# Kernel tuning notes

Hardware: AMD Instinct MI355X
Metric: run time of the kernel (lower is better)

Reference implementation:

```python
import jax, jax.numpy as jnp
import numpy as np

B, DIM, W0, H0 = 4, 256, 128, 128
HEADS, HEAD_DIM = 8, 32
FOLD, PROP = 2, 4
EPS_GN = 1e-5


def _l2norm(x):
    n = jnp.linalg.norm(x, axis=-1, keepdims=True)
    return x / jnp.maximum(n, 1e-12)  # matches F.normalize eps


def _fold(t, f):
    # (b, c, f*w, f*h) -> (b*f*f, c, w, h), matching einops '(b f1 f2)' ordering
    b, c, W, H = t.shape
    w, h = W // f, H // f
    return t.reshape(b, c, f, w, f, h).transpose(0, 2, 4, 1, 3, 5).reshape(b * f * f, c, w, h)


def _unfold(t, f, b0):
    bf, c, w, h = t.shape
    return t.reshape(b0, f, f, c, w, h).transpose(0, 3, 1, 4, 2, 5).reshape(b0, c, f * w, f * h)


def _pool(t, p):
    # AdaptiveAvgPool2d((p, p)) for divisible sizes
    b, c, w, h = t.shape
    return t.reshape(b, c, p, w // p, p, h // p).mean(axis=(3, 5))


def setup_inputs() -> dict:
    key = jax.random.key(0)
    ks = jax.random.split(key, 6)
    D = HEADS * HEAD_DIM
    return {
        "x": jax.random.normal(ks[0], (B, DIM, W0, H0), jnp.float32),
        "xyz": jax.random.normal(ks[1], (B, 3, W0, H0), jnp.float32),
        "Wv": jax.random.normal(ks[2], (D, DIM, 7, 7), jnp.float32) * 0.02,
        "bv": jnp.zeros((D,), jnp.float32),
        "Wproj": jax.random.normal(ks[3], (DIM, D), jnp.float32) * 0.02,
        "bproj": jnp.zeros((DIM,), jnp.float32),
        "gn_w": jnp.ones((D,), jnp.float32),
        "gn_b": jnp.zeros((D,), jnp.float32),
        "sim_alpha": jnp.ones((1,), jnp.float32),
        "sim_beta": jnp.zeros((1,), jnp.float32),
    }


def reference(x, xyz, Wv, bv, Wproj, bproj, gn_w, gn_b, sim_alpha, sim_beta):
    # value = self.v(x): 7x7 conv, padding 3
    value = jax.lax.conv_general_dilated(
        x, Wv, (1, 1), ((3, 3), (3, 3)),
        dimension_numbers=("NCHW", "OIHW", "NCHW")) + bv[None, :, None, None]
    b0 = x.shape[0]
    # heads split: 'b (e c) w h -> (b e) c w h'
    xh = x.reshape(b0 * HEADS, HEAD_DIM, W0, H0)
    vh = value.reshape(b0 * HEADS, HEAD_DIM, W0, H0)
    xf = _fold(xh, FOLD)
    vf = _fold(vh, FOLD)
    xyzf = _fold(xyz, FOLD)
    bb, c, w, h = xf.shape
    M = PROP * PROP
    N = w * h
    centers = _pool(xf, PROP)                                   # (bb, c, p, p)
    xyz_c = _pool(xyzf, PROP)
    value_centers = _pool(vf, PROP).reshape(bb, c, M).transpose(0, 2, 1)  # (bb, M, c)
    cen = centers.reshape(bb, c, M).transpose(0, 2, 1)          # (bb, M, c)
    xpts = xf.reshape(bb, c, N).transpose(0, 2, 1)              # (bb, N, c)
    vpts = vf.reshape(bb, c, N).transpose(0, 2, 1)              # (bb, N, c)
    sim = jax.nn.sigmoid(sim_beta + sim_alpha *
                         jnp.einsum('bmc,bnc->bmn', _l2norm(cen), _l2norm(xpts)))
    bg = xyzf.shape[0]
    xyz_pts = xyzf.reshape(bg, 3, N).transpose(0, 2, 1)
    xyz_cc = xyz_c.reshape(bg, 3, M).transpose(0, 2, 1)
    sim_geo = jax.nn.sigmoid(sim_beta + sim_alpha *
                             jnp.einsum('bmc,bnc->bmn', _l2norm(xyz_cc), _l2norm(xyz_pts)))
    sim_geo = jnp.tile(sim_geo, (sim.shape[0] // sim_geo.shape[0], 1, 1))  # torch .repeat
    sim = sim * sim_geo ** 2
    # faithful mask math: scatter_(1, argmax, 1.0) into an all-ones tensor leaves it all-ones,
    # so dense_mask == 1 and split_mask == 0 exactly as in the source.
    dense_mask = jnp.ones_like(sim)
    split_mask = 1.0 - dense_mask
    denss_sim = sim * dense_mask
    split_sim = sim * split_mask
    split_out = (jnp.einsum('bmn,bnc->bmc', split_sim, vpts) + value_centers) \
                / (split_sim.sum(-1, keepdims=True) + 1.0)
    denss_out = (jnp.einsum('bmn,bnc->bmc', denss_sim, xpts) + cen) \
                / (denss_sim.sum(-1, keepdims=True) + 1.0)
    denss_pts = jnp.einsum('bmc,bmn->bnc', denss_out, denss_sim)  # (bb, N, c)
    split_pts = jnp.einsum('bmc,bmn->bnc', split_out, split_sim)
    out = (denss_pts + split_pts).transpose(0, 2, 1).reshape(bb, c, w, h)
    out = _unfold(out, FOLD, b0 * HEADS)
    out = out.reshape(b0, HEADS * HEAD_DIM, W0, H0)
    # GroupNorm with 1 group: normalize over (C, H, W) per sample
    mu = out.mean(axis=(1, 2, 3), keepdims=True)
    var = ((out - mu) ** 2).mean(axis=(1, 2, 3), keepdims=True)
    out = (out - mu) / jnp.sqrt(var + EPS_GN)
    out = out * gn_w[None, :, None, None] + gn_b[None, :, None, None]
    # proj 1x1 conv + silu
    out = jnp.einsum('bchw,oc->bohw', out, Wproj) + bproj[None, :, None, None]
    return jax.nn.silu(out)
```

## Files before the change

### kernel.cpp

```cpp
#include <hip/hip_runtime.h>
#include <stdint.h>


typedef __attribute__((ext_vector_type(8))) short short8;
typedef __attribute__((ext_vector_type(4))) float floatx4;
typedef __fp16 fp16x2 __attribute__((ext_vector_type(2)));

#define SIMW 264

__device__ float g_sbp[256];
__device__ float g_bias[1024];
__device__ __attribute__((aligned(16))) _Float16 g_Wa[4*256*256];
__device__ float g_cenraw[128*16*32];
__device__ float g_cenhat[128*16*32];
__device__ float g_gcenhat[16*16*4];
__device__ __attribute__((aligned(16))) _Float16 g_sim[(size_t)128*4096*16];
__device__ float g_dnum[128*16*16*32];
__device__ float g_Gp[(size_t)128*16*256];
__device__ float g_rsum[128*16*16];
__device__ __attribute__((aligned(16))) unsigned g_dnh2[128*256];

static __device__ __forceinline__ fp16x2 as_h2(unsigned u) { return __builtin_bit_cast(fp16x2, u); }
static __device__ __forceinline__ unsigned pk(float a, float b) {
  return __builtin_bit_cast(unsigned, __builtin_amdgcn_cvt_pkrtz(a, b));
}
static __device__ __forceinline__ float h16(float v) {
  return (float)as_h2(pk(v, 0.f))[0];
}
#if __has_builtin(__builtin_amdgcn_fdot2)
static __device__ __forceinline__ float fdot2(fp16x2 a, fp16x2 b, float c) {
  return __builtin_amdgcn_fdot2(a, b, c, false);
}
#else
static __device__ __forceinline__ float fdot2(fp16x2 a, fp16x2 b, float c) {
  return c + (float)a[0]*(float)b[0] + (float)a[1]*(float)b[1];
}
#endif
static __device__ __forceinline__ float sum16(const float* p) {
  const float4* q = (const float4*)p;
  float4 a = q[0], b = q[1], c = q[2], d = q[3];
  return (a.x+a.y+a.z+a.w) + (b.x+b.y+b.z+b.w) + (c.x+c.y+c.z+c.w) + (d.x+d.y+d.z+d.w);
}
static __device__ __forceinline__ float sigm(float z) {
  return __builtin_amdgcn_rcpf(1.f + __expf(-z));
}

__global__ __launch_bounds__(128) void k01_pool(const float* __restrict__ x,
                                                const float* __restrict__ xyz) {
  __shared__ float cenL[128];
  __shared__ float invL[4];
  __shared__ float gc[64];
  const int blk = blockIdx.x;
  const int tid = threadIdx.x;
  if (blk < 512) {
    const int bb = blk >> 2, pi = blk & 3;
    const int b = bb >> 5, e = (bb >> 2) & 7, f1 = (bb >> 1) & 1, f2 = bb & 1;
    const int c = tid >> 2, pj = tid & 3;
    const int m = pi*4 + pj;
    const float* p = x + ((size_t)(b*256 + e*32 + c)*128 + f1*64 + pi*16)*128 + f2*64 + pj*16;
    float s = 0.f;
    #pragma unroll
    for (int r = 0; r < 16; ++r) s += sum16(p + r*128);
    const float raw = s * (1.f/256.f);
    cenL[pj*32 + c] = raw;
    g_cenraw[(bb*16 + m)*32 + c] = raw;
    __syncthreads();
    if (tid < 4) {
      float ss = 0.f;
      #pragma unroll
      for (int cc = 0; cc < 32; ++cc) { float v = cenL[tid*32+cc]; ss += v*v; }
      invL[tid] = 1.f / fmaxf(sqrtf(ss), 1e-12f);
    }
    __syncthreads();
    g_cenhat[(bb*16 + m)*32 + c] = raw * invL[pj];
  } else {
    const int gti = blk - 512;
    const int bg = gti >> 2, f1 = (gti >> 1) & 1, f2 = gti & 1;
    if (tid < 48) {
      const int m = tid / 3, ch = tid - 3*(tid/3);
      const int pi = m >> 2, pj = m & 3;
      const float* p = xyz + (size_t)(bg*3+ch)*16384 + (f1*64 + pi*16)*128 + f2*64 + pj*16;
      float s = 0.f;
      #pragma unroll
      for (int r = 0; r < 16; ++r) s += sum16(p + r*128);
      gc[m*4+ch] = s * (1.f/256.f);
    }
    __syncthreads();
    if (tid < 16) {
      float g0 = gc[tid*4], g1 = gc[tid*4+1], g2 = gc[tid*4+2];
      float inv = 1.f / fmaxf(sqrtf(g0*g0+g1*g1+g2*g2), 1e-12f);
      float* o = g_gcenhat + gti*64 + tid*4;
      o[0] = g0*inv; o[1] = g1*inv; o[2] = g2*inv; o[3] = 0.f;
    }
  }
}

__global__ __launch_bounds__(256, 5) void k1b_sim(const float* __restrict__ x,
                                                  const float* __restrict__ xyz,
                                                  const float* __restrict__ salpha,
                                                  const float* __restrict__ sbeta) {
  __shared__ __attribute__((aligned(16))) unsigned  xL[256*20];
  __shared__ __attribute__((aligned(16))) _Float16 simS[16*SIMW];
  __shared__ __attribute__((aligned(16))) unsigned chP[16*16];
  __shared__ float gcenL[64];
  __shared__ float rsW[64];
  float* ovl = (float*)xL;
  const int blk = blockIdx.x;
  const int bb = blk >> 4, ck = blk & 15;
  const int b = bb >> 5, e = (bb >> 2) & 7, f1 = (bb >> 1) & 1, f2 = bb & 1;
  const int gti = ((e & 3) << 2) | (f1 << 1) | f2;
  const int tid = threadIdx.x, lane = tid & 63, wave = tid >> 6;
  const int lm = lane & 15, quad = lane >> 4;
  const float alpha = salpha[0], beta = sbeta[0];
  const float* xt = x + (((size_t)(b*256 + e*32))*128 + f1*64)*128 + f2*64;

  {
    const float2 cp = *(const float2*)(g_cenhat + bb*512 + tid*2);
    chP[tid] = pk(cp.x, cp.y);
  }
  if (tid < 64) gcenL[tid] = g_gcenhat[gti*64 + tid];
  __syncthreads();

  const int ng = ck*256 + tid;
  const int wi = ng >> 6, hi = ng & 63;
  const int addr = wi*128 + hi;
  {
    float ss = 0.f;
    unsigned xp[16];
    #pragma unroll
    for (int p = 0; p < 16; ++p) {
      const float v0 = xt[(size_t)(2*p)*16384 + addr];
      const float v1 = xt[(size_t)(2*p+1)*16384 + addr];
      ss += v0*v0 + v1*v1;
      xp[p] = pk(v0, v1);
    }
    uint4 u0 = {xp[0],xp[1],xp[2],xp[3]};
    uint4 u1 = {xp[4],xp[5],xp[6],xp[7]};
    uint4 u2 = {xp[8],xp[9],xp[10],xp[11]};
    uint4 u3 = {xp[12],xp[13],xp[14],xp[15]};
    *(uint4*)(xL + tid*20)      = u0;
    *(uint4*)(xL + tid*20 + 4)  = u1;
    *(uint4*)(xL + tid*20 + 8)  = u2;
    *(uint4*)(xL + tid*20 + 12) = u3;
    const float invn = __builtin_amdgcn_rcpf(fmaxf(sqrtf(ss), 1e-12f));
    const float* gp = xyz + (size_t)((e & 3)*3)*16384 + (f1*64 + wi)*128 + f2*64 + hi;
    float g0 = gp[0], g1 = gp[16384], g2 = gp[32768];
    const float invg = __builtin_amdgcn_rcpf(fmaxf(sqrtf(g0*g0+g1*g1+g2*g2), 1e-12f));
    float4 tail = {invn, g0*invg, g1*invg, g2*invg};
    *(float4*)((float*)xL + tid*20 + 16) = tail;
  }
  __syncthreads();

  {
    const short8 afx = *(const short8*)((const _Float16*)chP + lm*32 + quad*8);
    float rsacc[4] = {0.f, 0.f, 0.f, 0.f};
    #pragma unroll
    for (int t = 0; t < 4; ++t) {
      const int px = wave*64 + t*16 + lm;
      const short8 bfx = *(const short8*)((const _Float16*)xL + px*40 + quad*8);
      floatx4 d = {0.f,0.f,0.f,0.f};
      d = __builtin_amdgcn_mfma_f32_16x16x32_f16(afx, bfx, d, 0, 0, 0);
      const float4 ig = *(const float4*)((const float*)xL + px*20 + 16);
      #pragma unroll
      for (int r = 0; r < 4; ++r) {
        const int m = quad*4 + r;
        const float* gh = gcenL + m*4;
        const float dg = gh[0]*ig.y + gh[1]*ig.z + gh[2]*ig.w;
        const float gg = sigm(beta + alpha*dg);
        const float sv = sigm(beta + alpha * d[r] * ig.x) * gg * gg;
        rsacc[r] += sv;
        simS[m*SIMW + px] = (_Float16)sv;
      }
    }
    #pragma unroll
    for (int r = 0; r < 4; ++r) {
      float v = rsacc[r];
      v += __shfl_xor(v, 1, 64); v += __shfl_xor(v, 2, 64);
      v += __shfl_xor(v, 4, 64); v += __shfl_xor(v, 8, 64);
      if (lm == 0) rsW[wave*16 + quad*4 + r] = v;
    }
  }
  __syncthreads();

  {
    unsigned w[8];
    const unsigned short* sp = (const unsigned short*)simS;
    #pragma unroll
    for (int p = 0; p < 8; ++p)
      w[p] = (unsigned)sp[(2*p)*SIMW + tid] | ((unsigned)sp[(2*p+1)*SIMW + tid] << 16);
    _Float16* gp = g_sim + ((size_t)bb*4096 + ng)*16;
    *(uint4*)gp       = *(const uint4*)&w[0];
    *(uint4*)(gp + 8) = *(const uint4*)&w[4];
  }
  if (tid < 16)
    g_rsum[(bb*16 + ck)*16 + tid] = rsW[tid] + rsW[16+tid] + rsW[32+tid] + rsW[48+tid];

  {
    floatx4 acc0 = {0.f,0.f,0.f,0.f}, acc1 = {0.f,0.f,0.f,0.f};
    floatx4 accG = {0.f,0.f,0.f,0.f};
    #pragma unroll
    for (int ks = 0; ks < 2; ++ks) {
      const int kb = wave*64 + ks*32 + quad*8;
      const short8 af = *(const short8*)(simS + lm*SIMW + kb);
      const int ag = ck*512 + ((kb >> 6)*128) + (kb & 63);
      const float* pb0 = xt + (size_t)lm*16384 + ag;
      const float* pb1 = pb0 + (size_t)16*16384;
      short8 bf0, bf1;
      #pragma unroll
      for (int t = 0; t < 8; ++t) bf0[t] = __builtin_bit_cast(short, (_Float16)pb0[t]);
      #pragma unroll
      for (int t = 0; t < 8; ++t) bf1[t] = __builtin_bit_cast(short, (_Float16)pb1[t]);
      acc0 = __builtin_amdgcn_mfma_f32_16x16x32_f16(af, bf0, acc0, 0, 0, 0);
      acc1 = __builtin_amdgcn_mfma_f32_16x16x32_f16(af, bf1, acc1, 0, 0, 0);
      accG = __builtin_amdgcn_mfma_f32_16x16x32_f16(af, af,  accG, 0, 0, 0);
    }
    #pragma unroll
    for (int r = 0; r < 4; ++r) {
      const int m = quad*4 + r;
      ovl[wave*512 + m*32 + lm]        = acc0[r];
      ovl[wave*512 + m*32 + 16 + lm]   = acc1[r];
      ovl[2048 + wave*256 + m*16 + lm] = accG[r];
    }
  }
  __syncthreads();

  {
    const float d0 = ovl[tid]       + ovl[512 + tid]  + ovl[1024 + tid] + ovl[1536 + tid];
    const float d1 = ovl[256 + tid] + ovl[768 + tid]  + ovl[1280 + tid] + ovl[1792 + tid];
    g_dnum[(size_t)(bb*16 + ck)*512 + tid]       = d0;
    g_dnum[(size_t)(bb*16 + ck)*512 + 256 + tid] = d1;
    const float gsum = ovl[2048 + tid] + ovl[2304 + tid] + ovl[2560 + tid] + ovl[2816 + tid];
    g_Gp[(size_t)(bb*16 + ck)*256 + tid] = gsum;
  }
}

__global__ __launch_bounds__(512) void k1c_red() {
  __shared__ float denssL[512];
  __shared__ float rsL[16];
  __shared__ float red[16];
  const int bb = blockIdx.x, tid = threadIdx.x, lane = tid & 63, wv = tid >> 6;
  if (tid < 16) {
    float r = 1.f;
    #pragma unroll
    for (int k = 0; k < 16; ++k) r += g_rsum[(bb*16 + k)*16 + tid];
    rsL[tid] = r;
  }
  float a = g_cenraw[bb*512 + tid];
  #pragma unroll
  for (int k = 0; k < 16; ++k) a += g_dnum[(size_t)bb*8192 + k*512 + tid];
  __syncthreads();
  denssL[tid] = a / rsL[tid >> 5];
  __syncthreads();
  if (tid < 256) {
    const int c = tid >> 3, mp = tid & 7;
    g_dnh2[bb*256 + c*8 + mp] = pk(denssL[(2*mp)*32 + c], denssL[(2*mp+1)*32 + c]);
  }
  float contrib = 0.f;
  if (tid < 256) {
    const int m = tid >> 4, m2 = tid & 15;
    float g = 0.f;
    #pragma unroll
    for (int k = 0; k < 16; ++k) g += g_Gp[((size_t)bb*16 + k)*256 + tid];
    float p = 0.f;
    #pragma unroll
    for (int c = 0; c < 32; ++c)
      p += h16(denssL[m*32 + c]) * h16(denssL[m2*32 + c]);
    contrib = g * p;
  }
  float s1t = 0.f;
  if (tid < 16) {
    float sc = 0.f;
    #pragma unroll
    for (int c = 0; c < 32; ++c) sc += h16(denssL[tid*32 + c]);
    s1t = (rsL[tid] - 1.f) * sc;
  }
  #pragma unroll
  for (int off = 1; off < 64; off <<= 1) {
    contrib += __shfl_xor(contrib, off, 64);
    s1t     += __shfl_xor(s1t, off, 64);
  }
  if (lane == 0) { red[wv] = contrib; red[8 + wv] = s1t; }
  __syncthreads();
  if (tid == 0) {
    float s2 = 0.f, s1 = 0.f;
    #pragma unroll
    for (int w = 0; w < 8; ++w) { s2 += red[w]; s1 += red[8 + w]; }
    g_sbp[bb*2]     = s1;
    g_sbp[bb*2 + 1] = s2;
  }
}

__global__ __launch_bounds__(256) void k2_prep(const float* __restrict__ Wp,
                                               const float* __restrict__ bpr,
                                               const float* __restrict__ gnw,
                                               const float* __restrict__ gnb) {
  __shared__ float betaL[256];
  __shared__ float alphaL[256];
  __shared__ float S12[2];
  const int b = blockIdx.x, t = threadIdx.x;
  if (t < 64) {
    float v1 = 0.f, v2 = 0.f;
    if (t < 32) { v1 = g_sbp[(b*32 + t)*2]; v2 = g_sbp[(b*32 + t)*2 + 1]; }
    #pragma unroll
    for (int off = 1; off < 64; off <<= 1) { v1 += __shfl_xor(v1, off, 64); v2 += __shfl_xor(v2, off, 64); }
    if (t == 0) { S12[0] = v1; S12[1] = v2; }
  }
  __syncthreads();
  const float S1 = S12[0];
  const float S2 = S12[1];
  const float inv_n = 1.f / 4194304.f;
  const float mu  = S1 * inv_n;
  const float inv = rsqrtf(fmaxf(S2*inv_n - mu*mu, 0.f) + 1e-5f);
  const float a = inv * gnw[t];
  alphaL[t] = a;
  betaL[t] = gnb[t] - mu * a;
  __syncthreads();
  float k = bpr[t];
  const float* wr = Wp + t*256;
  _Float16* wa = g_Wa + ((size_t)b*256 + t)*256;
  for (int c = 0; c < 256; c += 8) {
    const float4 w0 = *(const float4*)(wr + c);
    const float4 w1 = *(const float4*)(wr + c + 4);
    k += w0.x*betaL[c+0] + w0.y*betaL[c+1] + w0.z*betaL[c+2] + w0.w*betaL[c+3]
       + w1.x*betaL[c+4] + w1.y*betaL[c+5] + w1.z*betaL[c+6] + w1.w*betaL[c+7];
    uint4 o;
    o.x = pk(w0.x*alphaL[c+0], w0.y*alphaL[c+1]);
    o.y = pk(w0.z*alphaL[c+2], w0.w*alphaL[c+3]);
    o.z = pk(w1.x*alphaL[c+4], w1.y*alphaL[c+5]);
    o.w = pk(w1.z*alphaL[c+6], w1.w*alphaL[c+7]);
    *(uint4*)(wa + c) = o;
  }
  g_bias[b*256 + t] = k;
}

__global__ __launch_bounds__(256, 4) void kf_proj(float* __restrict__ out) {
  __shared__ __attribute__((aligned(16))) _Float16 preL[64*256];
  __shared__ float biasL[256];
  const int blk = blockIdx.x;
  const int b = blk >> 8, pb = blk & 255;
  const int f1 = pb >> 7, f2 = pb & 1;
  const int nbase = ((pb >> 1) & 63) * 64;
  const int tid = threadIdx.x, lane = tid & 63, wave = tid >> 6;
  const int lm = lane & 15, quad = lane >> 4;
  const int m0 = wave*64;
  biasL[tid] = g_bias[b*256 + tid];

  #pragma unroll
  for (int eh = 0; eh < 2; ++eh) {
    const int e = wave*2 + eh;
    const int bb = b*32 + e*4 + f1*2 + f2;
    short8 bf0 = {}, bf1 = {};
    if (quad < 2) {
      const _Float16* dp = (const _Float16*)g_dnh2 + (size_t)bb*512 + quad*8;
      bf0 = *(const short8*)(dp + lm*16);
      bf1 = *(const short8*)(dp + (16 + lm)*16);
    }
    #pragma unroll
    for (int pt = 0; pt < 4; ++pt) {
      const short8 af = *(const short8*)(g_sim
          + ((size_t)bb*4096 + nbase + pt*16 + lm)*16 + (quad & 1)*8);
      floatx4 c0 = {0.f,0.f,0.f,0.f}, c1 = {0.f,0.f,0.f,0.f};
      c0 = __builtin_amdgcn_mfma_f32_16x16x32_f16(af, bf0, c0, 0, 0, 0);
      c1 = __builtin_amdgcn_mfma_f32_16x16x32_f16(af, bf1, c1, 0, 0, 0);
      #pragma unroll
      for (int r = 0; r < 4; ++r) {
        const int px = pt*16 + quad*4 + r;
        const int swz = (px & 7) << 4;
        const int b0 = (px*512 + (e*32 + lm)*2) ^ swz;
        const int b1 = (px*512 + (e*32 + 16 + lm)*2) ^ swz;
        *(_Float16*)((char*)preL + b0) = (_Float16)c0[r];
        *(_Float16*)((char*)preL + b1) = (_Float16)c1[r];
      }
    }
  }
  __syncthreads();

  floatx4 acc[4][4] = {};
  #pragma unroll
  for (int ks = 0; ks < 8; ++ks) {
    const _Float16* abase = g_Wa + ((size_t)b*256)*256 + (size_t)ks*32 + quad*8;
    short8 afr[4], bfr[4];
    #pragma unroll
    for (int mi = 0; mi < 4; ++mi)
      afr[mi] = *(const short8*)(abase + (size_t)(m0 + mi*16 + lm)*256);
    #pragma unroll
    for (int ni = 0; ni < 4; ++ni) {
      const int row = ni*16 + lm;
      const int byte = (row*512 + ks*64 + quad*16) ^ ((row & 7) << 4);
      bfr[ni] = *(const short8*)((const char*)preL + byte);
    }
    #pragma unroll
    for (int mi = 0; mi < 4; ++mi) {
      #pragma unroll
      for (int ni = 0; ni < 4; ++ni)
        acc[mi][ni] = __builtin_amdgcn_mfma_f32_16x16x32_f16(afr[mi], bfr[ni], acc[mi][ni], 0, 0, 0);
    }
  }
  #pragma unroll
  for (int mi = 0; mi < 4; ++mi) {
    #pragma unroll
    for (int r = 0; r < 4; ++r) {
      const int o = m0 + mi*16 + quad*4 + r;
      const float kb = biasL[o];
      #pragma unroll
      for (int ni = 0; ni < 4; ++ni) {
        float val = acc[mi][ni][r] + kb;
        val = val * sigm(val);
        out[((size_t)(b*256 + o))*16384 + pb*64 + ni*16 + lm] = val;
      }
    }
  }
}

extern "C" void kernel_launch(void* const* d_in, const int* in_sizes, int n_in,
                              void* d_out, int out_size, void* d_ws, size_t ws_size,
                              hipStream_t stream)
{
  (void)in_sizes; (void)n_in; (void)d_ws; (void)ws_size; (void)out_size;
  const float* x     = (const float*)d_in[0];
  const float* xyz   = (const float*)d_in[1];
  const float* Wproj = (const float*)d_in[4];
  const float* bproj = (const float*)d_in[5];
  const float* gnw   = (const float*)d_in[6];
  const float* gnb   = (const float*)d_in[7];
  const float* sa    = (const float*)d_in[8];
  const float* sb    = (const float*)d_in[9];
  float* out = (float*)d_out;

  hipLaunchKernelGGL(k01_pool, dim3(528),  dim3(128), 0, stream, x, xyz);
  hipLaunchKernelGGL(k1b_sim,  dim3(2048), dim3(256), 0, stream, x, xyz, sa, sb);
  hipLaunchKernelGGL(k1c_red,  dim3(128),  dim3(512), 0, stream);
  hipLaunchKernelGGL(k2_prep,  dim3(4),    dim3(256), 0, stream, Wproj, bproj, gnw, gnb);
  hipLaunchKernelGGL(kf_proj,  dim3(1024), dim3(256), 0, stream, out);
}
```

Measured before the change: 235.2 us.

## Fold dense centers into projection weights to shrink final GEMM K dimension

The projection weights are premultiplied by the per-head dense center features (W_eff = Wproj·alpha·dnum) in the prep kernel. The final kernel can then multiply W_eff directly by the similarity matrix with K=128 instead of 256, which removes the intermediate pre-projection MFMA stage and its LDS staging. The prep kernel grows from 4 to 16 blocks and writes per-fold effective weights. This adds another fp16 rounding of the fused weights, which may change accuracy slightly.

Result: faster. 228.3 us (-2.9%).

```diff
diff --git a/kernel.cpp b/kernel.cpp
--- a/kernel.cpp
+++ b/kernel.cpp
@@ -10,7 +10,6 @@
 
 __device__ float g_sbp[256];
 __device__ float g_bias[1024];
-__device__ __attribute__((aligned(16))) _Float16 g_Wa[4*256*256];
 __device__ float g_cenraw[128*16*32];
 __device__ float g_cenhat[128*16*32];
 __device__ float g_gcenhat[16*16*4];
@@ -19,6 +18,7 @@
 __device__ float g_Gp[(size_t)128*16*256];
 __device__ float g_rsum[128*16*16];
 __device__ __attribute__((aligned(16))) unsigned g_dnh2[128*256];
+__device__ __attribute__((aligned(16))) _Float16 g_Weff[(size_t)16*256*128];
 
 static __device__ __forceinline__ fp16x2 as_h2(unsigned u) { return __builtin_bit_cast(fp16x2, u); }
 static __device__ __forceinline__ unsigned pk(float a, float b) {
@@ -252,8 +252,8 @@
   denssL[tid] = a / rsL[tid >> 5];
   __syncthreads();
   if (tid < 256) {
-    const int c = tid >> 3, mp = tid & 7;
-    g_dnh2[bb*256 + c*8 + mp] = pk(denssL[(2*mp)*32 + c], denssL[(2*mp+1)*32 + c]);
+    const int m = tid >> 4, cp = tid & 15;
+    g_dnh2[bb*256 + m*16 + cp] = pk(denssL[m*32 + 2*cp], denssL[m*32 + 2*cp + 1]);
   }
   float contrib = 0.f;
   if (tid < 256) {
@@ -290,14 +290,17 @@
   }
 }
 
-__global__ __launch_bounds__(256) void k2_prep(const float* __restrict__ Wp,
-                                               const float* __restrict__ bpr,
-                                               const float* __restrict__ gnw,
-                                               const float* __restrict__ gnb) {
+__global__ __launch_bounds__(256) void k2w_prep(const float* __restrict__ Wp,
+                                                const float* __restrict__ bpr,
+                                                const float* __restrict__ gnw,
+                                                const float* __restrict__ gnb) {
+  __shared__ float alphaL[256];
   __shared__ float betaL[256];
-  __shared__ float alphaL[256];
   __shared__ float S12[2];
-  const int b = blockIdx.x, t = threadIdx.x;
+  __shared__ unsigned dh[8*256];
+  const int blk = blockIdx.x;
+  const int b = blk >> 2, q = blk & 3;
+  const int t = threadIdx.x;
   if (t < 64) {
     float v1 = 0.f, v2 = 0.f;
     if (t < 32) { v1 = g_sbp[(b*32 + t)*2]; v2 = g_sbp[(b*32 + t)*2 + 1]; }
@@ -305,90 +308,87 @@
     for (int off = 1; off < 64; off <<= 1) { v1 += __shfl_xor(v1, off, 64); v2 += __shfl_xor(v2, off, 64); }
     if (t == 0) { S12[0] = v1; S12[1] = v2; }
   }
+  #pragma unroll
+  for (int e = 0; e < 8; ++e)
+    dh[e*256 + t] = g_dnh2[(b*32 + e*4 + q)*256 + t];
   __syncthreads();
   const float S1 = S12[0];
   const float S2 = S12[1];
   const float inv_n = 1.f / 4194304.f;
   const float mu  = S1 * inv_n;
   const float inv = rsqrtf(fmaxf(S2*inv_n - mu*mu, 0.f) + 1e-5f);
-  const float a = inv * gnw[t];
-  alphaL[t] = a;
-  betaL[t] = gnb[t] - mu * a;
-  __syncthreads();
-  float k = bpr[t];
+  const float aa = inv * gnw[t];
+  alphaL[t] = aa;
+  betaL[t] = gnb[t] - mu * aa;
+  __syncthreads();
+
+  float kacc = bpr[t];
   const float* wr = Wp + t*256;
-  _Float16* wa = g_Wa + ((size_t)b*256 + t)*256;
-  for (int c = 0; c < 256; c += 8) {
-    const float4 w0 = *(const float4*)(wr + c);
-    const float4 w1 = *(const float4*)(wr + c + 4);
-    k += w0.x*betaL[c+0] + w0.y*betaL[c+1] + w0.z*betaL[c+2] + w0.w*betaL[c+3]
-       + w1.x*betaL[c+4] + w1.y*betaL[c+5] + w1.z*betaL[c+6] + w1.w*betaL[c+7];
-    uint4 o;
-    o.x = pk(w0.x*alphaL[c+0], w0.y*alphaL[c+1]);
-    o.y = pk(w0.z*alphaL[c+2], w0.w*alphaL[c+3]);
-    o.z = pk(w1.x*alphaL[c+4], w1.y*alphaL[c+5]);
-    o.w = pk(w1.z*alphaL[c+6], w1.w*alphaL[c+7]);
-    *(uint4*)(wa + c) = o;
-  }
-  g_bias[b*256 + t] = k;
+  _Float16* wo = g_Weff + ((size_t)blk*256 + t)*128;
+  #pragma unroll
+  for (int e = 0; e < 8; ++e) {
+    float w[32];
+    #pragma unroll
+    for (int c8 = 0; c8 < 4; ++c8) {
+      const float4 wv0 = *(const float4*)(wr + e*32 + c8*8);
+      const float4 wv1 = *(const float4*)(wr + e*32 + c8*8 + 4);
+      w[c8*8+0]=wv0.x; w[c8*8+1]=wv0.y; w[c8*8+2]=wv0.z; w[c8*8+3]=wv0.w;
+      w[c8*8+4]=wv1.x; w[c8*8+5]=wv1.y; w[c8*8+6]=wv1.z; w[c8*8+7]=wv1.w;
+    }
+    unsigned wap[16];
+    #pragma unroll
+    for (int p = 0; p < 16; ++p) {
+      const int C = e*32 + 2*p;
+      kacc += w[2*p]*betaL[C] + w[2*p+1]*betaL[C+1];
+      wap[p] = pk(w[2*p]*alphaL[C], w[2*p+1]*alphaL[C+1]);
+    }
+    const unsigned* dm = dh + e*256;
+    float weff[16];
+    #pragma unroll
+    for (int m = 0; m < 16; ++m) {
+      float s = 0.f;
+      #pragma unroll
+      for (int cp = 0; cp < 16; ++cp)
+        s = fdot2(as_h2(dm[m*16 + cp]), as_h2(wap[cp]), s);
+      weff[m] = s;
+    }
+    uint4 o0, o1;
+    o0.x = pk(weff[0],weff[1]);   o0.y = pk(weff[2],weff[3]);
+    o0.z = pk(weff[4],weff[5]);   o0.w = pk(weff[6],weff[7]);
+    o1.x = pk(weff[8],weff[9]);   o1.y = pk(weff[10],weff[11]);
+    o1.z = pk(weff[12],weff[13]); o1.w = pk(weff[14],weff[15]);
+    *(uint4*)(wo + e*16)     = o0;
+    *(uint4*)(wo + e*16 + 8) = o1;
+  }
+  if (q == 0) g_bias[b*256 + t] = kacc;
 }
 
 __global__ __launch_bounds__(256, 4) void kf_proj(float* __restrict__ out) {
-  __shared__ __attribute__((aligned(16))) _Float16 preL[64*256];
   __shared__ float biasL[256];
   const int blk = blockIdx.x;
   const int b = blk >> 8, pb = blk & 255;
-  const int f1 = pb >> 7, f2 = pb & 1;
+  const int q = ((pb >> 7) << 1) | (pb & 1);
   const int nbase = ((pb >> 1) & 63) * 64;
   const int tid = threadIdx.x, lane = tid & 63, wave = tid >> 6;
   const int lm = lane & 15, quad = lane >> 4;
   const int m0 = wave*64;
   biasL[tid] = g_bias[b*256 + tid];
-
-  #pragma unroll
-  for (int eh = 0; eh < 2; ++eh) {
-    const int e = wave*2 + eh;
-    const int bb = b*32 + e*4 + f1*2 + f2;
-    short8 bf0 = {}, bf1 = {};
-    if (quad < 2) {
-      const _Float16* dp = (const _Float16*)g_dnh2 + (size_t)bb*512 + quad*8;
-      bf0 = *(const short8*)(dp + lm*16);
-      bf1 = *(const short8*)(dp + (16 + lm)*16);
-    }
-    #pragma unroll
-    for (int pt = 0; pt < 4; ++pt) {
-      const short8 af = *(const short8*)(g_sim
-          + ((size_t)bb*4096 + nbase + pt*16 + lm)*16 + (quad & 1)*8);
-      floatx4 c0 = {0.f,0.f,0.f,0.f}, c1 = {0.f,0.f,0.f,0.f};
-      c0 = __builtin_amdgcn_mfma_f32_16x16x32_f16(af, bf0, c0, 0, 0, 0);
-      c1 = __builtin_amdgcn_mfma_f32_16x16x32_f16(af, bf1, c1, 0, 0, 0);
-      #pragma unroll
-      for (int r = 0; r < 4; ++r) {
-        const int px = pt*16 + quad*4 + r;
-        const int swz = (px & 7) << 4;
-        const int b0 = (px*512 + (e*32 + lm)*2) ^ swz;
-        const int b1 = (px*512 + (e*32 + 16 + lm)*2) ^ swz;
-        *(_Float16*)((char*)preL + b0) = (_Float16)c0[r];
-        *(_Float16*)((char*)preL + b1) = (_Float16)c1[r];
-      }
-    }
-  }
-  __syncthreads();
-
+  __syncthreads();
+
+  const _Float16* wbase = g_Weff + ((size_t)(b*4 + q)*256)*128;
   floatx4 acc[4][4] = {};
   #pragma unroll
-  for (int ks = 0; ks < 8; ++ks) {
-    const _Float16* abase = g_Wa + ((size_t)b*256)*256 + (size_t)ks*32 + quad*8;
+  for (int ks = 0; ks < 4; ++ks) {
+    const int e  = ks*2 + (quad >> 1);
+    const int bbk = b*32 + e*4 + q;
+    const _Float16* sp = g_sim + ((size_t)bbk*4096 + nbase)*16 + (quad & 1)*8;
     short8 afr[4], bfr[4];
     #pragma unroll
     for (int mi = 0; mi < 4; ++mi)
-      afr[mi] = *(const short8*)(abase + (size_t)(m0 + mi*16 + lm)*256);
-    #pragma unroll
-    for (int ni = 0; ni < 4; ++ni) {
-      const int row = ni*16 + lm;
-      const int byte = (row*512 + ks*64 + quad*16) ^ ((row & 7) << 4);
-      bfr[ni] = *(const short8*)((const char*)preL + byte);
-    }
+      afr[mi] = *(const short8*)(wbase + (size_t)(m0 + mi*16 + lm)*128 + ks*32 + quad*8);
+    #pragma unroll
+    for (int ni = 0; ni < 4; ++ni)
+      bfr[ni] = *(const short8*)(sp + (ni*16 + lm)*16);
     #pragma unroll
     for (int mi = 0; mi < 4; ++mi) {
       #pragma unroll
@@ -430,6 +430,6 @@
   hipLaunchKernelGGL(k01_pool, dim3(528),  dim3(128), 0, stream, x, xyz);
   hipLaunchKernelGGL(k1b_sim,  dim3(2048), dim3(256), 0, stream, x, xyz, sa, sb);
   hipLaunchKernelGGL(k1c_red,  dim3(128),  dim3(512), 0, stream);
-  hipLaunchKernelGGL(k2_prep,  dim3(4),    dim3(256), 0, stream, Wproj, bproj, gnw, gnb);
+  hipLaunchKernelGGL(k2w_prep, dim3(16),   dim3(256), 0, stream, Wproj, bproj, gnw, gnb);
   hipLaunchKernelGGL(kf_proj,  dim3(1024), dim3(256), 0, stream, out);
 }
```
